# Optimization experiments

Hardware: AMD Instinct MI355X
Metric: run time of the kernel (lower is better)

The kernel has to match this reference:

```python
import jax, jax.numpy as jnp
import numpy as np

B, S, D, H, F = 8, 1024, 1024, 16, 4096
DH = D // H  # 64
EPS = 1e-5


def layer_norm(x, g, b):
    mu = jnp.mean(x, axis=-1, keepdims=True)
    var = jnp.mean(jnp.square(x - mu), axis=-1, keepdims=True)
    return (x - mu) * jax.lax.rsqrt(var + EPS) * g + b


def mha(q_in, k_in, v_in, wq, wk, wv, wo, causal):
    # wq/wk/wv: [H, D, DH] (stacked per-head nn.Linear weights, pre-transposed)
    Q = jnp.einsum('bsd,hdk->bhsk', q_in, wq)
    K = jnp.einsum('bsd,hdk->bhsk', k_in, wk)
    V = jnp.einsum('bsd,hdk->bhsk', v_in, wv)
    scores = jnp.einsum('bhsk,bhtk->bhst', Q, K) / jnp.sqrt(jnp.asarray(DH, Q.dtype))
    if causal:
        mask = jnp.triu(jnp.ones((S, S), dtype=bool), k=1)  # True = inaccessible
        scores = jnp.where(mask, -jnp.inf, scores)
    A = jax.nn.softmax(scores, axis=-1)
    heads = jnp.einsum('bhst,bhtk->bhsk', A, V)
    heads = heads.transpose(0, 2, 1, 3).reshape(q_in.shape[0], q_in.shape[1], D)
    return heads @ wo.T  # nn.Linear convention


def setup_inputs() -> dict:
    key = jax.random.key(0)
    ks = jax.random.split(key, 16)
    sc = 1.0 / np.sqrt(D)
    scf = 1.0 / np.sqrt(F)
    return {
        'embeds': jax.random.normal(ks[0], (B, S, D), jnp.float32),
        'encoder_output': jax.random.normal(ks[1], (B, S, D), jnp.float32),
        'wq1': jax.random.normal(ks[2], (H, D, DH), jnp.float32) * sc,
        'wk1': jax.random.normal(ks[3], (H, D, DH), jnp.float32) * sc,
        'wv1': jax.random.normal(ks[4], (H, D, DH), jnp.float32) * sc,
        'wo1': jax.random.normal(ks[5], (D, D), jnp.float32) * sc,
        'wq2': jax.random.normal(ks[6], (H, D, DH), jnp.float32) * sc,
        'wk2': jax.random.normal(ks[7], (H, D, DH), jnp.float32) * sc,
        'wv2': jax.random.normal(ks[8], (H, D, DH), jnp.float32) * sc,
        'wo2': jax.random.normal(ks[9], (D, D), jnp.float32) * sc,
        'ln1_g': jnp.ones((D,), jnp.float32), 'ln1_b': jnp.zeros((D,), jnp.float32),
        'ln2_g': jnp.ones((D,), jnp.float32), 'ln2_b': jnp.zeros((D,), jnp.float32),
        'ln3_g': jnp.ones((D,), jnp.float32), 'ln3_b': jnp.zeros((D,), jnp.float32),
        'w1': jax.random.normal(ks[10], (F, D), jnp.float32) * sc,
        'b1': jnp.zeros((F,), jnp.float32),
        'w2': jax.random.normal(ks[11], (D, F), jnp.float32) * scf,
        'b2': jnp.zeros((D,), jnp.float32),
    }


def reference(embeds, encoder_output, wq1, wk1, wv1, wo1, wq2, wk2, wv2, wo2,
              ln1_g, ln1_b, ln2_g, ln2_b, ln3_g, ln3_b, w1, b1, w2, b2):
    # masked (causal) self-attention + residual + LN
    sa = mha(embeds, embeds, embeds, wq1, wk1, wv1, wo1, causal=True)
    x1 = layer_norm(sa + embeds, ln1_g, ln1_b)
    # cross-attention (no mask) + residual + LN
    ca = mha(x1, encoder_output, encoder_output, wq2, wk2, wv2, wo2, causal=False)
    x2 = layer_norm(ca + x1, ln2_g, ln2_b)
    # feedforward (Linear -> GELU(exact) -> Linear) + residual + LN
    ff = jax.nn.gelu(x2 @ w1.T + b1, approximate=False) @ w2.T + b2
    return layer_norm(ff + x2, ln3_g, ln3_b)
```

## Files before the change

kernel.cpp:

```cpp
#include <hip/hip_runtime.h>
#include <cstdint>
#include <cstddef>

typedef unsigned short u16;
typedef __attribute__((ext_vector_type(4))) float f32x4;
typedef __attribute__((ext_vector_type(4))) float f4;
typedef __attribute__((ext_vector_type(8))) short short8x;
typedef __attribute__((ext_vector_type(4))) u16 u16x4;
typedef __attribute__((ext_vector_type(8))) u16 u16x8;

#define DEV static __device__ __forceinline__

DEV void gl_lds16(const void* g, void* l) {
  __builtin_amdgcn_global_load_lds(
      (const __attribute__((address_space(1))) unsigned int*)g,
      (__attribute__((address_space(3))) unsigned int*)l, 16, 0, 0);
}

DEV u16 f2bf(float f) {
  unsigned u = __float_as_uint(f);
  u += 0x7fffu + ((u >> 16) & 1u);
  return (u16)(u >> 16);
}


__global__ __launch_bounds__(256) void cast_bf16(const float* __restrict__ X, u16* __restrict__ Y) {
  size_t i = ((size_t)blockIdx.x * 256 + threadIdx.x) * 4;
  f4 v = *(const f4*)(X + i);
  u16x4 y;
#pragma unroll
  for (int j = 0; j < 4; ++j) y[j] = f2bf(v[j]);
  *(u16x4*)(Y + i) = y;
}

__global__ __launch_bounds__(256) void cast_wqkv(const float* __restrict__ W, u16* __restrict__ Wt) {
  __shared__ float tile[64][65];
  const int t = threadIdx.x;
  const int h = blockIdx.y;
  const int d0 = blockIdx.x * 64;
  const float* Wb = W + (size_t)h * (1024 * 64);
  const int di = t >> 2;
  const int j0 = (t & 3) * 16;
#pragma unroll
  for (int c = 0; c < 4; ++c) {
    f4 v = *(const f4*)(Wb + (size_t)(d0 + di) * 64 + j0 + c * 4);
#pragma unroll
    for (int j = 0; j < 4; ++j) tile[di][j0 + c * 4 + j] = v[j];
  }
  __syncthreads();
  const int k = t >> 2;
  const int dd0 = (t & 3) * 16;
  u16x8 o0, o1;
#pragma unroll
  for (int u = 0; u < 8; ++u) o0[u] = f2bf(tile[dd0 + u][k]);
#pragma unroll
  for (int u = 0; u < 8; ++u) o1[u] = f2bf(tile[dd0 + 8 + u][k]);
  u16* dst = Wt + (size_t)(h * 64 + k) * 1024 + d0 + dd0;
  *(u16x8*)(dst) = o0;
  *(u16x8*)(dst + 8) = o1;
}

__global__ __launch_bounds__(256) void transpose_v(const u16* __restrict__ V, u16* __restrict__ Vt,
                                                   int vstride, int voff) {
  __shared__ u16 tile[32][72];
  const int t = threadIdx.x;
  const int bh = blockIdx.y;
  const int s0 = blockIdx.x * 32;
  const u16* Vb = V + (size_t)(bh >> 4) * (1024 * (size_t)vstride) + voff + (bh & 15) * 64;
  const int si = t >> 3, d0 = (t & 7) * 8;
  u16x8 val = *(const u16x8*)(Vb + (size_t)(s0 + si) * vstride + d0);
#pragma unroll
  for (int u = 0; u < 8; ++u) tile[si][d0 + u] = val[u];
  __syncthreads();
  const int d = t >> 2, sj0 = (t & 3) * 8;
  u16x8 o;
#pragma unroll
  for (int u = 0; u < 8; ++u) o[u] = tile[sj0 + u][d];
  *(u16x8*)(Vt + (size_t)bh * (64 * 1024) + (size_t)d * 1024 + s0 + sj0) = o;
}

template <int EPI>
__global__ __launch_bounds__(256, 3) void gemm_bt(const u16* __restrict__ A, const u16* __restrict__ Bt,
                                                  void* __restrict__ C, const float* __restrict__ bias,
                                                  int K, int ldc) {
  __shared__ u16 As0[128 * 32], Bs0[128 * 32];
  __shared__ u16 As1[128 * 32], Bs1[128 * 32];
  const int t = threadIdx.x;
  const int wave = t >> 6, lane = t & 63;
  const int lr = lane & 15, lkg = lane >> 4;
  const int swz = (lr >> 1) & 3;
  const int wr = (wave >> 1) * 64, wc = (wave & 1) * 64;

  const int gx = gridDim.x;
  const int nwg = gx * gridDim.y;
  const int flat = blockIdx.y * gx + blockIdx.x;
  const int wg = (flat & 7) * (nwg >> 3) + (flat >> 3);
  const int m0 = (wg / gx) * 128, n0 = (wg % gx) * 128;

  const int schunk = ((t & 3) ^ ((t >> 3) & 3)) << 4;
  const size_t rowskip = (size_t)64 * K * 2;
  const char* gA0 = (const char*)(A + (size_t)(m0 + (t >> 2)) * K) + schunk;
  const char* gA1 = gA0 + rowskip;
  const char* gB0 = (const char*)(Bt + (size_t)(n0 + (t >> 2)) * K) + schunk;
  const char* gB1 = gB0 + rowskip;

  char* dA0 = (char*)As0 + wave * 1024;
  char* dB0 = (char*)Bs0 + wave * 1024;
  char* dA1 = (char*)As1 + wave * 1024;
  char* dB1 = (char*)Bs1 + wave * 1024;

  const int aoff = (wr + lr) * 64 + ((lkg ^ swz) << 4);
  const int boff = (wc + lr) * 64 + ((lkg ^ swz) << 4);
  const char* rA0 = (const char*)As0 + aoff;
  const char* rB0 = (const char*)Bs0 + boff;
  const char* rA1 = (const char*)As1 + aoff;
  const char* rB1 = (const char*)Bs1 + boff;

  const f32x4 fzero = {0.f, 0.f, 0.f, 0.f};
  f32x4 acc[4][4];
#pragma unroll
  for (int m = 0; m < 4; ++m)
#pragma unroll
    for (int n = 0; n < 4; ++n) acc[m][n] = fzero;

  auto compute = [&](const char* rA, const char* rB) {
    short8x aF[4], bF[4];
#pragma unroll
    for (int m = 0; m < 4; ++m) aF[m] = *(const short8x*)(rA + m * 1024);
#pragma unroll
    for (int n = 0; n < 4; ++n) bF[n] = *(const short8x*)(rB + n * 1024);
#pragma unroll
    for (int m = 0; m < 4; ++m)
#pragma unroll
      for (int n = 0; n < 4; ++n)
        acc[m][n] = __builtin_amdgcn_mfma_f32_16x16x32_bf16(aF[m], bF[n], acc[m][n], 0, 0, 0);
  };

  gl_lds16(gA0, dA0); gl_lds16(gA1, dA0 + 4096);
  gl_lds16(gB0, dB0); gl_lds16(gB1, dB0 + 4096);
  gA0 += 64; gA1 += 64; gB0 += 64; gB1 += 64;
  __syncthreads();

  const int nk2 = K >> 6;
  for (int p = 0; p < nk2; ++p) {
    gl_lds16(gA0, dA1); gl_lds16(gA1, dA1 + 4096);
    gl_lds16(gB0, dB1); gl_lds16(gB1, dB1 + 4096);
    gA0 += 64; gA1 += 64; gB0 += 64; gB1 += 64;
    compute(rA0, rB0);
    __syncthreads();
    if (p + 1 < nk2) {
      gl_lds16(gA0, dA0); gl_lds16(gA1, dA0 + 4096);
      gl_lds16(gB0, dB0); gl_lds16(gB1, dB0 + 4096);
    }
    gA0 += 64; gA1 += 64; gB0 += 64; gB1 += 64;
    compute(rA1, rB1);
    __syncthreads();
  }

#pragma unroll
  for (int m = 0; m < 4; ++m) {
#pragma unroll
    for (int rr = 0; rr < 4; ++rr) {
      const int gm = m0 + wr + m * 16 + lkg * 4 + rr;
#pragma unroll
      for (int n = 0; n < 4; ++n) {
        const int gn = n0 + wc + n * 16 + lr;
        float v = acc[m][n][rr];
        if (EPI == 2 || EPI == 3) v += bias[gn];
        if (EPI == 2) v = 0.5f * v * (1.0f + erff(v * 0.70710678118654752f));
        if (EPI == 4) v *= 0.125f;
        if (EPI == 5 && gn < 1024) v *= 0.125f;
        if (EPI == 1 || EPI == 3)
          ((float*)C)[(size_t)gm * ldc + gn] = v;
        else
          ((u16*)C)[(size_t)gm * ldc + gn] = f2bf(v);
      }
    }
  }
}

template <int CAUSAL>
__global__ __launch_bounds__(256, 2) void flash_attn(const u16* __restrict__ Q, const u16* __restrict__ Kk,
                                                     const u16* __restrict__ Vt, u16* __restrict__ O,
                                                     int qst) {
  __shared__ u16 Ks[2][64 * 64];
  __shared__ u16 Vs[2][64 * 64];
  __shared__ u16 Ps[4][32 * 72];
  const int t = threadIdx.x;
  const int wave = t >> 6, lane = t & 63;
  const int lr = lane & 15, lkg = lane >> 4, lk = lkg * 8;
  const int sw = lr & 7;
  const int bh = blockIdx.y;
  const size_t base = (size_t)(bh >> 4) * (1024 * (size_t)qst) + (bh & 15) * 64;
  const u16* Qb = Q + base;
  const u16* Kb = Kk + base;
  const u16* Vtb = Vt + (size_t)bh * (64 * 1024);
  u16* Ob = O + (size_t)(bh >> 4) * (1024 * 1024) + (bh & 15) * 64;
  const int qt = blockIdx.x * 128;
  const int qw = qt + wave * 32;

  const f32x4 fzero = {0.f, 0.f, 0.f, 0.f};
  short8x qf[2][2];
#pragma unroll
  for (int rb = 0; rb < 2; ++rb)
#pragma unroll
    for (int kk = 0; kk < 2; ++kk)
      qf[rb][kk] = *(const short8x*)(Qb + (size_t)(qw + rb * 16 + lr) * qst + kk * 32 + lk);

  float m_[2][4], l_[2][4];
  f32x4 o_[2][4];
#pragma unroll
  for (int rb = 0; rb < 2; ++rb) {
#pragma unroll
    for (int rr = 0; rr < 4; ++rr) { m_[rb][rr] = -1e30f; l_[rb][rr] = 0.f; }
#pragma unroll
    for (int db = 0; db < 4; ++db) o_[rb][db] = fzero;
  }

  const int rsel = lane >> 3;
  const int csw = ((lane & 7) ^ rsel) << 4;

  auto stage = [&](int buf, int kv0) {
#pragma unroll
    for (int s = 0; s < 2; ++s) {
      const int row = s * 32 + wave * 8 + rsel;
      gl_lds16((const char*)Kb + (size_t)(kv0 + row) * (size_t)(qst * 2) + csw,
               (char*)&Ks[buf][0] + s * 4096 + wave * 1024);
      gl_lds16((const char*)Vtb + (size_t)row * 2048 + (size_t)kv0 * 2 + csw,
               (char*)&Vs[buf][0] + s * 4096 + wave * 1024);
    }
  };

  const int kv_end = CAUSAL ? (qt + 128) : 1024;
  const int nt = kv_end >> 6;

  stage(0, 0);
  __syncthreads();
  int cur = 0;
  for (int tt = 0; tt < nt; ++tt) {
    const int kv0 = tt * 64;
    if (tt + 1 < nt) stage(cur ^ 1, kv0 + 64);

    const char* ksb = (const char*)&Ks[cur][0];
    const char* vsb = (const char*)&Vs[cur][0];

    short8x kf[4][2];
#pragma unroll
    for (int nb = 0; nb < 4; ++nb) {
      const int row = nb * 16 + lr;
#pragma unroll
      for (int kk = 0; kk < 2; ++kk)
        kf[nb][kk] = *(const short8x*)(ksb + row * 128 + (((kk * 4 + lkg) ^ sw) << 4));
    }

#pragma unroll
    for (int rb = 0; rb < 2; ++rb) {
      f32x4 s[4];
#pragma unroll
      for (int nb = 0; nb < 4; ++nb) {
        s[nb] = __builtin_amdgcn_mfma_f32_16x16x32_bf16(qf[rb][0], kf[nb][0], fzero, 0, 0, 0);
        s[nb] = __builtin_amdgcn_mfma_f32_16x16x32_bf16(qf[rb][1], kf[nb][1], s[nb], 0, 0, 0);
      }
      if (CAUSAL && (kv0 + 63 > qw + rb * 16)) {
#pragma unroll
        for (int rr = 0; rr < 4; ++rr) {
          const int qg = qw + rb * 16 + lkg * 4 + rr;
#pragma unroll
          for (int nb = 0; nb < 4; ++nb)
            if (kv0 + nb * 16 + lr > qg) s[nb][rr] = -1e30f;
        }
      }
#pragma unroll
      for (int rr = 0; rr < 4; ++rr) {
        float mx = fmaxf(fmaxf(s[0][rr], s[1][rr]), fmaxf(s[2][rr], s[3][rr]));
#pragma unroll
        for (int d = 1; d < 16; d <<= 1) mx = fmaxf(mx, __shfl_xor(mx, d, 16));
        const float mold = m_[rb][rr];
        const float mnew = fmaxf(mold, mx);
        float p[4];
#pragma unroll
        for (int nb = 0; nb < 4; ++nb) p[nb] = __expf(s[nb][rr] - mnew);
        float rsum = (p[0] + p[1]) + (p[2] + p[3]);
#pragma unroll
        for (int d = 1; d < 16; d <<= 1) rsum += __shfl_xor(rsum, d, 16);
        const float alpha = __expf(mold - mnew);
        m_[rb][rr] = mnew;
        l_[rb][rr] = l_[rb][rr] * alpha + rsum;
#pragma unroll
        for (int db = 0; db < 4; ++db) o_[rb][db][rr] *= alpha;
        const int prow = rb * 16 + lkg * 4 + rr;
#pragma unroll
        for (int nb = 0; nb < 4; ++nb)
          Ps[wave][prow * 72 + nb * 16 + lr] = f2bf(p[nb]);
      }
    }
    asm volatile("s_waitcnt lgkmcnt(0)" ::: "memory");

    short8x vF[4][2];
#pragma unroll
    for (int db = 0; db < 4; ++db) {
      const int row = db * 16 + lr;
#pragma unroll
      for (int kk = 0; kk < 2; ++kk)
        vF[db][kk] = *(const short8x*)(vsb + row * 128 + (((kk * 4 + lkg) ^ sw) << 4));
    }
#pragma unroll
    for (int rb = 0; rb < 2; ++rb) {
#pragma unroll
      for (int kk = 0; kk < 2; ++kk) {
        const short8x aP = *(const short8x*)((const char*)&Ps[wave][0] + (rb * 16 + lr) * 144 + kk * 64 + lkg * 16);
#pragma unroll
        for (int db = 0; db < 4; ++db)
          o_[rb][db] = __builtin_amdgcn_mfma_f32_16x16x32_bf16(aP, vF[db][kk], o_[rb][db], 0, 0, 0);
      }
    }
    __syncthreads();
    cur ^= 1;
  }

#pragma unroll
  for (int rb = 0; rb < 2; ++rb)
#pragma unroll
    for (int rr = 0; rr < 4; ++rr) {
      const float inv = 1.0f / l_[rb][rr];
      const int qg = qw + rb * 16 + lkg * 4 + rr;
#pragma unroll
      for (int db = 0; db < 4; ++db)
        Ob[(size_t)qg * 1024 + db * 16 + lr] = f2bf(o_[rb][db][rr] * inv);
    }
}

__global__ __launch_bounds__(256) void ln_res(const float* __restrict__ X, const float* __restrict__ bias,
                                              const float* __restrict__ R,
                                              const float* __restrict__ gam, const float* __restrict__ bet,
                                              float* __restrict__ oF, u16* __restrict__ oB) {
  __shared__ float red[8];
  const int row = blockIdx.x, t = threadIdx.x;
  const int wave = t >> 6, lane = t & 63;
  const size_t off = (size_t)row * 1024 + t * 4;
  f4 x = *(const f4*)(X + off);
  f4 r = *(const f4*)(R + off);
  float v[4];
#pragma unroll
  for (int j = 0; j < 4; ++j) v[j] = x[j] + r[j];
  if (bias) {
    f4 bb = *(const f4*)(bias + t * 4);
#pragma unroll
    for (int j = 0; j < 4; ++j) v[j] += bb[j];
  }
  float s = 0.f, sq = 0.f;
#pragma unroll
  for (int j = 0; j < 4; ++j) { s += v[j]; sq += v[j] * v[j]; }
#pragma unroll
  for (int d = 1; d < 64; d <<= 1) {
    s += __shfl_xor(s, d, 64);
    sq += __shfl_xor(sq, d, 64);
  }
  if (lane == 0) { red[wave * 2] = s; red[wave * 2 + 1] = sq; }
  __syncthreads();
  s = red[0] + red[2] + red[4] + red[6];
  sq = red[1] + red[3] + red[5] + red[7];
  const float mu = s * (1.0f / 1024.0f);
  const float var = sq * (1.0f / 1024.0f) - mu * mu;
  const float rs = rsqrtf(var + 1e-5f);
  f4 g4 = *(const f4*)(gam + t * 4);
  f4 b4 = *(const f4*)(bet + t * 4);
  f4 y;
#pragma unroll
  for (int j = 0; j < 4; ++j) y[j] = (v[j] - mu) * rs * g4[j] + b4[j];
  *(f4*)(oF + off) = y;
  if (oB) {
    u16x4 yb;
#pragma unroll
    for (int j = 0; j < 4; ++j) yb[j] = f2bf(y[j]);
    *(u16x4*)(oB + off) = yb;
  }
}

extern "C" void kernel_launch(void* const* d_in, const int* in_sizes, int n_in,
                              void* d_out, int out_size, void* d_ws, size_t ws_size,
                              hipStream_t stream) {
  const float* embeds = (const float*)d_in[0];
  const float* enc = (const float*)d_in[1];
  const float* wq1 = (const float*)d_in[2];
  const float* wk1 = (const float*)d_in[3];
  const float* wv1 = (const float*)d_in[4];
  const float* wo1 = (const float*)d_in[5];
  const float* wq2 = (const float*)d_in[6];
  const float* wk2 = (const float*)d_in[7];
  const float* wv2 = (const float*)d_in[8];
  const float* wo2 = (const float*)d_in[9];
  const float* ln1g = (const float*)d_in[10];
  const float* ln1b = (const float*)d_in[11];
  const float* ln2g = (const float*)d_in[12];
  const float* ln2b = (const float*)d_in[13];
  const float* ln3g = (const float*)d_in[14];
  const float* ln3b = (const float*)d_in[15];
  const float* w1 = (const float*)d_in[16];
  const float* b1 = (const float*)d_in[17];
  const float* w2 = (const float*)d_in[18];
  const float* b2 = (const float*)d_in[19];
  float* out = (float*)d_out;
  char* ws = (char*)d_ws;
  const size_t MB = (size_t)1 << 20;

  u16* QKV = (u16*)(ws + 0 * MB);
  u16* Vtb = (u16*)(ws + 48 * MB);
  u16* Hd = (u16*)(ws + 64 * MB);
  float* Of = (float*)(ws + 80 * MB);
  u16* ebf = (u16*)(ws + 112 * MB);
  u16* encb = (u16*)(ws + 128 * MB);
  float* x1f = (float*)(ws + 144 * MB);
  float* x2f = (float*)(ws + 176 * MB);
  u16* Wq1t = (u16*)(ws + 208 * MB);
  u16* Wk1t = (u16*)(ws + 210 * MB);
  u16* Wv1t = (u16*)(ws + 212 * MB);
  u16* Wo1b = (u16*)(ws + 214 * MB);
  u16* Wq2t = (u16*)(ws + 216 * MB);
  u16* Wk2t = (u16*)(ws + 218 * MB);
  u16* Wv2t = (u16*)(ws + 220 * MB);
  u16* Wo2b = (u16*)(ws + 222 * MB);
  u16* W1b = (u16*)(ws + 224 * MB);
  u16* W2b = (u16*)(ws + 232 * MB);
  u16* x1b = ebf;
  u16* x2b = encb;
  u16* Hff = (u16*)(ws + 0 * MB);

  dim3 blk(256);

  cast_bf16<<<8192, blk, 0, stream>>>(embeds, ebf);
  cast_bf16<<<8192, blk, 0, stream>>>(enc, encb);
  cast_wqkv<<<dim3(16, 16), blk, 0, stream>>>(wq1, Wq1t);
  cast_wqkv<<<dim3(16, 16), blk, 0, stream>>>(wk1, Wk1t);
  cast_wqkv<<<dim3(16, 16), blk, 0, stream>>>(wv1, Wv1t);
  cast_wqkv<<<dim3(16, 16), blk, 0, stream>>>(wq2, Wq2t);
  cast_wqkv<<<dim3(16, 16), blk, 0, stream>>>(wk2, Wk2t);
  cast_wqkv<<<dim3(16, 16), blk, 0, stream>>>(wv2, Wv2t);
  cast_bf16<<<1024, blk, 0, stream>>>(wo1, Wo1b);
  cast_bf16<<<1024, blk, 0, stream>>>(wo2, Wo2b);
  cast_bf16<<<4096, blk, 0, stream>>>(w1, W1b);
  cast_bf16<<<4096, blk, 0, stream>>>(w2, W2b);

  gemm_bt<5><<<dim3(24, 64), blk, 0, stream>>>(ebf, Wq1t, QKV, nullptr, 1024, 3072);
  transpose_v<<<dim3(32, 128), blk, 0, stream>>>(QKV, Vtb, 3072, 2048);
  flash_attn<1><<<dim3(8, 128), blk, 0, stream>>>(QKV, QKV + 1024, Vtb, Hd, 3072);
  gemm_bt<1><<<dim3(8, 64), blk, 0, stream>>>(Hd, Wo1b, Of, nullptr, 1024, 1024);
  ln_res<<<8192, blk, 0, stream>>>(Of, nullptr, embeds, ln1g, ln1b, x1f, x1b);

  gemm_bt<4><<<dim3(8, 64), blk, 0, stream>>>(x1b, Wq2t, QKV, nullptr, 1024, 3072);
  gemm_bt<0><<<dim3(16, 64), blk, 0, stream>>>(encb, Wk2t, QKV + 1024, nullptr, 1024, 3072);
  transpose_v<<<dim3(32, 128), blk, 0, stream>>>(QKV, Vtb, 3072, 2048);
  flash_attn<0><<<dim3(8, 128), blk, 0, stream>>>(QKV, QKV + 1024, Vtb, Hd, 3072);
  gemm_bt<1><<<dim3(8, 64), blk, 0, stream>>>(Hd, Wo2b, Of, nullptr, 1024, 1024);
  ln_res<<<8192, blk, 0, stream>>>(Of, nullptr, x1f, ln2g, ln2b, x2f, x2b);

  gemm_bt<2><<<dim3(32, 64), blk, 0, stream>>>(x2b, W1b, Hff, b1, 1024, 4096);
  gemm_bt<3><<<dim3(8, 64), blk, 0, stream>>>(Hff, W2b, Of, b2, 4096, 1024);
  ln_res<<<8192, blk, 0, stream>>>(Of, nullptr, x2f, ln3g, ln3b, out, nullptr);
}
```

Before: 719.5 us.

## Split-K the N=1024 GEMMs and reduce partials inside the residual LayerNorm

The output-projection and FF2 GEMMs gain a grid z dimension that splits K into two halves. Each half writes its own fp32 partial buffer. The following ln_res kernel takes a second input and sums the partials, and for FF2 the bias add also moves there. The aim is to double the number of workgroups for these 8x64-tile GEMMs, which underfill the GPU, at the cost of extra fp32 partial writes and reads.

```diff
diff --git a/kernel.cpp b/kernel.cpp
--- a/kernel.cpp
+++ b/kernel.cpp
@@ -82,7 +82,7 @@
 template <int EPI>
 __global__ __launch_bounds__(256, 3) void gemm_bt(const u16* __restrict__ A, const u16* __restrict__ Bt,
                                                   void* __restrict__ C, const float* __restrict__ bias,
-                                                  int K, int ldc) {
+                                                  int Krow, int Kit, int ldc, long long zC) {
   __shared__ u16 As0[128 * 32], Bs0[128 * 32];
   __shared__ u16 As1[128 * 32], Bs1[128 * 32];
   const int t = threadIdx.x;
@@ -98,10 +98,12 @@
   const int m0 = (wg / gx) * 128, n0 = (wg % gx) * 128;
 
   const int schunk = ((t & 3) ^ ((t >> 3) & 3)) << 4;
-  const size_t rowskip = (size_t)64 * K * 2;
-  const char* gA0 = (const char*)(A + (size_t)(m0 + (t >> 2)) * K) + schunk;
+  const size_t rowb = (size_t)Krow * 2;
+  const size_t rowskip = (size_t)64 * rowb;
+  const size_t zoff = (size_t)blockIdx.z * (size_t)Kit * 2;
+  const char* gA0 = (const char*)A + (size_t)(m0 + (t >> 2)) * rowb + zoff + schunk;
   const char* gA1 = gA0 + rowskip;
-  const char* gB0 = (const char*)(Bt + (size_t)(n0 + (t >> 2)) * K) + schunk;
+  const char* gB0 = (const char*)Bt + (size_t)(n0 + (t >> 2)) * rowb + zoff + schunk;
   const char* gB1 = gB0 + rowskip;
 
   char* dA0 = (char*)As0 + wave * 1024;
@@ -141,7 +143,7 @@
   gA0 += 64; gA1 += 64; gB0 += 64; gB1 += 64;
   __syncthreads();
 
-  const int nk2 = K >> 6;
+  const int nk2 = Kit >> 6;
   for (int p = 0; p < nk2; ++p) {
     gl_lds16(gA0, dA1); gl_lds16(gA1, dA1 + 4096);
     gl_lds16(gB0, dB1); gl_lds16(gB1, dB1 + 4096);
@@ -171,7 +173,7 @@
         if (EPI == 4) v *= 0.125f;
         if (EPI == 5 && gn < 1024) v *= 0.125f;
         if (EPI == 1 || EPI == 3)
-          ((float*)C)[(size_t)gm * ldc + gn] = v;
+          ((float*)C)[(size_t)blockIdx.z * zC + (size_t)gm * ldc + gn] = v;
         else
           ((u16*)C)[(size_t)gm * ldc + gn] = f2bf(v);
       }
@@ -330,8 +332,8 @@
     }
 }
 
-__global__ __launch_bounds__(256) void ln_res(const float* __restrict__ X, const float* __restrict__ bias,
-                                              const float* __restrict__ R,
+__global__ __launch_bounds__(256) void ln_res(const float* __restrict__ X, const float* __restrict__ X2,
+                                              const float* __restrict__ bias, const float* __restrict__ R,
                                               const float* __restrict__ gam, const float* __restrict__ bet,
                                               float* __restrict__ oF, u16* __restrict__ oB) {
   __shared__ float red[8];
@@ -343,6 +345,11 @@
   float v[4];
 #pragma unroll
   for (int j = 0; j < 4; ++j) v[j] = x[j] + r[j];
+  if (X2) {
+    f4 x2 = *(const f4*)(X2 + off);
+#pragma unroll
+    for (int j = 0; j < 4; ++j) v[j] += x2[j];
+  }
   if (bias) {
     f4 bb = *(const f4*)(bias + t * 4);
 #pragma unroll
@@ -426,6 +433,10 @@
   u16* x2b = encb;
   u16* Hff = (u16*)(ws + 0 * MB);
 
+  float* P0 = (float*)(ws + 0 * MB);
+  float* P3 = (float*)(ws + 112 * MB);
+  const long long ZC = (long long)8192 * 1024;
+
   dim3 blk(256);
 
   cast_bf16<<<8192, blk, 0, stream>>>(embeds, ebf);
@@ -441,20 +452,20 @@
   cast_bf16<<<4096, blk, 0, stream>>>(w1, W1b);
   cast_bf16<<<4096, blk, 0, stream>>>(w2, W2b);
 
-  gemm_bt<5><<<dim3(24, 64), blk, 0, stream>>>(ebf, Wq1t, QKV, nullptr, 1024, 3072);
+  gemm_bt<5><<<dim3(24, 64), blk, 0, stream>>>(ebf, Wq1t, QKV, nullptr, 1024, 1024, 3072, 0);
   transpose_v<<<dim3(32, 128), blk, 0, stream>>>(QKV, Vtb, 3072, 2048);
   flash_attn<1><<<dim3(8, 128), blk, 0, stream>>>(QKV, QKV + 1024, Vtb, Hd, 3072);
-  gemm_bt<1><<<dim3(8, 64), blk, 0, stream>>>(Hd, Wo1b, Of, nullptr, 1024, 1024);
-  ln_res<<<8192, blk, 0, stream>>>(Of, nullptr, embeds, ln1g, ln1b, x1f, x1b);
-
-  gemm_bt<4><<<dim3(8, 64), blk, 0, stream>>>(x1b, Wq2t, QKV, nullptr, 1024, 3072);
-  gemm_bt<0><<<dim3(16, 64), blk, 0, stream>>>(encb, Wk2t, QKV + 1024, nullptr, 1024, 3072);
+  gemm_bt<1><<<dim3(8, 64, 2), blk, 0, stream>>>(Hd, Wo1b, P0, nullptr, 1024, 512, 1024, ZC);
+  ln_res<<<8192, blk, 0, stream>>>(P0, P0 + ZC, nullptr, embeds, ln1g, ln1b, x1f, x1b);
+
+  gemm_bt<4><<<dim3(8, 64), blk, 0, stream>>>(x1b, Wq2t, QKV, nullptr, 1024, 1024, 3072, 0);
+  gemm_bt<0><<<dim3(16, 64), blk, 0, stream>>>(encb, Wk2t, QKV + 1024, nullptr, 1024, 1024, 3072, 0);
   transpose_v<<<dim3(32, 128), blk, 0, stream>>>(QKV, Vtb, 3072, 2048);
   flash_attn<0><<<dim3(8, 128), blk, 0, stream>>>(QKV, QKV + 1024, Vtb, Hd, 3072);
-  gemm_bt<1><<<dim3(8, 64), blk, 0, stream>>>(Hd, Wo2b, Of, nullptr, 1024, 1024);
-  ln_res<<<8192, blk, 0, stream>>>(Of, nullptr, x1f, ln2g, ln2b, x2f, x2b);
-
-  gemm_bt<2><<<dim3(32, 64), blk, 0, stream>>>(x2b, W1b, Hff, b1, 1024, 4096);
-  gemm_bt<3><<<dim3(8, 64), blk, 0, stream>>>(Hff, W2b, Of, b2, 4096, 1024);
-  ln_res<<<8192, blk, 0, stream>>>(Of, nullptr, x2f, ln3g, ln3b, out, nullptr);
-}
+  gemm_bt<1><<<dim3(8, 64, 2), blk, 0, stream>>>(Hd, Wo2b, P0, nullptr, 1024, 512, 1024, ZC);
+  ln_res<<<8192, blk, 0, stream>>>(P0, P0 + ZC, nullptr, x1f, ln2g, ln2b, x2f, x2b);
+
+  gemm_bt<2><<<dim3(32, 64), blk, 0, stream>>>(x2b, W1b, Hff, b1, 1024, 1024, 4096, 0);
+  gemm_bt<1><<<dim3(8, 64, 2), blk, 0, stream>>>(Hff, W2b, Of, nullptr, 4096, 2048, 1024, ZC);
+  ln_res<<<8192, blk, 0, stream>>>(Of, P3, b2, x2f, ln3g, ln3b, out, nullptr);
+}
```

Result: no change. 725.5 us (+0.8%).
